# Kernel tuning notes

Measured on AMD Instinct MI355X. Metric: run time of the kernel, lower is better.

Reference implementation:

```python
import jax, jax.numpy as jnp
import numpy as np

N = 100000        # nodes
E = 3200000       # edges (avg degree 32)
F_IN = 512        # input node features
HIDDEN = 16       # hardcoded in GCN.__init__
NUM_CLASSES = 40


def setup_inputs() -> dict:
    key = jax.random.key(0)
    k1, k2, k3, k4 = jax.random.split(key, 4)
    edge_index = jax.random.randint(k1, (2, E), 0, N, dtype=jnp.int32)
    x = jax.random.normal(k2, (N, F_IN), dtype=jnp.float32)
    # GCNConv weights (glorot-ish scale) and biases
    W1 = jax.random.normal(k3, (F_IN, HIDDEN), dtype=jnp.float32) * (1.0 / np.sqrt(F_IN))
    b1 = jnp.zeros((HIDDEN,), dtype=jnp.float32)
    W2 = jax.random.normal(k4, (HIDDEN, NUM_CLASSES), dtype=jnp.float32) * (1.0 / np.sqrt(HIDDEN))
    b2 = jnp.zeros((NUM_CLASSES,), dtype=jnp.float32)
    return {"edge_index": edge_index, "x": x, "W1": W1, "b1": b1, "W2": W2, "b2": b2}


def _gcn_conv(x, src, dst, W, b, n):
    # PyG GCNConv: linear transform, symmetric-normalized scatter-add aggregation
    h = x @ W                                             # [N, out]
    deg = jax.ops.segment_sum(jnp.ones_like(dst, dtype=h.dtype), dst, num_segments=n)
    dinv = jnp.where(deg > 0, jax.lax.rsqrt(deg), 0.0)    # deg^{-1/2}
    norm = dinv[src] * dinv[dst]                          # [E_total]
    out = jax.ops.segment_sum(h[src] * norm[:, None], dst, num_segments=n)
    return out + b


def reference(edge_index, x, W1, b1, W2, b2):
    n = x.shape[0]
    # GCNConv adds self-loops by default
    loop = jnp.arange(n, dtype=edge_index.dtype)
    src = jnp.concatenate([edge_index[0], loop])
    dst = jnp.concatenate([edge_index[1], loop])
    h = _gcn_conv(x, src, dst, W1, b1, n)
    h = jax.nn.relu(h)
    # F.dropout(training=self.training) -> identity in eval mode
    h = _gcn_conv(h, src, dst, W2, b2, n)
    return jax.nn.log_softmax(h, axis=1)[::20]
```

## Files before the change

### kernel.cpp

```cpp
#include <hip/hip_runtime.h>
#include <cstdint>
#include <math.h>

#define F_IN 512
#define HID  16
#define NCLS 40
#define OUT_STRIDE 20
#define TB   256
#define NBA  256

typedef __attribute__((ext_vector_type(8))) short short8;
typedef __attribute__((ext_vector_type(4))) float f32x4;

__device__ inline unsigned short f2bf(float f) {
    unsigned u = __float_as_uint(f);
    u += 0x7fff + ((u >> 16) & 1);
    return (unsigned short)(u >> 16);
}
__device__ inline float bf2f(unsigned short h) {
    return __uint_as_float(((unsigned)h) << 16);
}

__global__ __launch_bounds__(256) void k_a1(const int* __restrict__ dst,
                                            int* __restrict__ cnt,
                                            int E, int NB, int chunk) {
    __shared__ int h[512];
    int t = threadIdx.x;
    for (int b = t; b < NB; b += 256) h[b] = 0;
    __syncthreads();
    int e0 = blockIdx.x * chunk, e1 = min(E, e0 + chunk);
    for (int e = e0 + t; e < e1; e += 256) {
        int d = __builtin_nontemporal_load(&dst[e]);
        atomicAdd(&h[d >> 8], 1);
    }
    __syncthreads();
    for (int b = t; b < NB; b += 256) cnt[(size_t)blockIdx.x * NB + b] = h[b];
}

__global__ __launch_bounds__(NBA) void k_a2a(const int* __restrict__ cnt,
                                             int* __restrict__ offsT,
                                             int* __restrict__ total, int NB) {
    __shared__ int s[NBA];
    int t = threadIdx.x, b = blockIdx.x;
    int v = cnt[(size_t)t * NB + b];
    s[t] = v;
    __syncthreads();
    for (int off = 1; off < NBA; off <<= 1) {
        int tmp = (t >= off) ? s[t - off] : 0;
        __syncthreads();
        s[t] += tmp;
        __syncthreads();
    }
    offsT[(size_t)b * NBA + t] = s[t] - v;
    if (t == NBA - 1) total[b] = s[t];
}

__global__ void k_a2bw(const int* __restrict__ total, int* __restrict__ base, int NB,
                       const float* __restrict__ W1, uint4* __restrict__ bfragg) {
    __shared__ int s[1024];
    int t = threadIdx.x;
    int v = (t < NB) ? total[t] : 0;
    s[t] = v;
    __syncthreads();
    for (int off = 1; off < 1024; off <<= 1) {
        int tmp = (t >= off) ? s[t - off] : 0;
        __syncthreads();
        s[t] += tmp;
        __syncthreads();
    }
    if (t < NB) base[t] = s[t] - v;
    if (t == NB - 1) base[NB] = s[t];

    int kstep = t >> 6, ln = t & 63;
    int col = ln & 15, k0 = kstep * 32 + (ln >> 4) * 8;
    unsigned up[4];
#pragma unroll
    for (int i = 0; i < 4; i++) {
        float a = W1[(k0 + 2 * i) * HID + col];
        float b = W1[(k0 + 2 * i + 1) * HID + col];
        up[i] = (unsigned)f2bf(a) | ((unsigned)f2bf(b) << 16);
    }
    bfragg[t] = make_uint4(up[0], up[1], up[2], up[3]);
}

__global__ __launch_bounds__(256) void k_a3(const int* __restrict__ src,
                                            const int* __restrict__ dst,
                                            const int* __restrict__ offsT,
                                            const int* __restrict__ base,
                                            unsigned* __restrict__ bin,
                                            int E, int NB, int chunk) {
    __shared__ int pos[512];
    int t = threadIdx.x, blk = blockIdx.x;
    for (int b = t; b < NB; b += 256) pos[b] = base[b] + offsT[(size_t)b * NBA + blk];
    __syncthreads();
    int e0 = blk * chunk, e1 = min(E, e0 + chunk);
    for (int e = e0 + t; e < e1; e += 256) {
        int d = __builtin_nontemporal_load(&dst[e]);
        int s = __builtin_nontemporal_load(&src[e]);
        int p = atomicAdd(&pos[d >> 8], 1);
        bin[p] = ((unsigned)s << 8) | (unsigned)(d & (TB - 1));
    }
}

__global__ __launch_bounds__(256) void k_sortb(const unsigned* __restrict__ bin,
                                               const int* __restrict__ base,
                                               int* __restrict__ csr,
                                               int* __restrict__ roff,
                                               float* __restrict__ dinv, int N) {
    __shared__ int cnt[TB], incl[TB], pos[TB];
    int t = threadIdx.x, b = blockIdx.x;
    cnt[t] = 0;
    __syncthreads();
    int j0 = base[b], j1 = base[b + 1];
    for (int j = j0 + t; j < j1; j += 256)
        atomicAdd(&cnt[bin[j] & (TB - 1)], 1);
    __syncthreads();
    incl[t] = cnt[t];
    __syncthreads();
    for (int off = 1; off < TB; off <<= 1) {
        int v = (t >= off) ? incl[t - off] : 0;
        __syncthreads();
        incl[t] += v;
        __syncthreads();
    }
    int ex = incl[t] - cnt[t];
    pos[t] = ex;
    int node = b * TB + t;
    if (node < N) {
        roff[node] = j0 + ex;
        dinv[node] = rsqrtf((float)cnt[t] + 1.0f);
    } else if (node == N) {
        roff[N] = j0 + ex;
    }
    __syncthreads();
    for (int j = j0 + t; j < j1; j += 256) {
        unsigned v = bin[j];
        int p = atomicAdd(&pos[v & (TB - 1)], 1);
        csr[j0 + p] = (int)(v >> 8);
    }
}

__global__ __launch_bounds__(64) void k_gemm1m(const float* __restrict__ x,
                                               const uint4* __restrict__ bfragg,
                                               const float* __restrict__ dinv,
                                               unsigned short* __restrict__ h1b, int n) {
    int lane = threadIdx.x;
    int rows0 = blockIdx.x * 64;
    int arow = lane & 15, kgrp = lane >> 4;

    const float* xr[4];
#pragma unroll
    for (int rt = 0; rt < 4; rt++) {
        int r = rows0 + rt * 16 + arow;
        if (r >= n) r = n - 1;
        xr[rt] = x + (size_t)r * F_IN + kgrp * 8;
    }

    f32x4 acc[4];
#pragma unroll
    for (int rt = 0; rt < 4; rt++) acc[rt] = (f32x4){0.f, 0.f, 0.f, 0.f};

#pragma unroll 4
    for (int kstep = 0; kstep < 16; kstep++) {
        uint4 braw = bfragg[kstep * 64 + lane];
        short8 b;
        *(uint4*)&b = braw;
#pragma unroll
        for (int rt = 0; rt < 4; rt++) {
            float4 lo = *(const float4*)(xr[rt] + kstep * 32);
            float4 hi = *(const float4*)(xr[rt] + kstep * 32 + 4);
            short8 a;
            a[0] = (short)f2bf(lo.x); a[1] = (short)f2bf(lo.y);
            a[2] = (short)f2bf(lo.z); a[3] = (short)f2bf(lo.w);
            a[4] = (short)f2bf(hi.x); a[5] = (short)f2bf(hi.y);
            a[6] = (short)f2bf(hi.z); a[7] = (short)f2bf(hi.w);
            acc[rt] = __builtin_amdgcn_mfma_f32_16x16x32_bf16(a, b, acc[rt], 0, 0, 0);
        }
    }

    int col = lane & 15, rbase = (lane >> 4) * 4;
#pragma unroll
    for (int rt = 0; rt < 4; rt++) {
#pragma unroll
        for (int r = 0; r < 4; r++) {
            int row = rows0 + rt * 16 + rbase + r;
            if (row < n)
                h1b[(size_t)row * HID + col] = f2bf(acc[rt][r] * dinv[row]);
        }
    }
}

__global__ __launch_bounds__(256) void k_agg(const unsigned* __restrict__ h1u,
                                             const int* __restrict__ csr,
                                             const int* __restrict__ roff,
                                             const float* __restrict__ dinv,
                                             const float* __restrict__ b1,
                                             unsigned* __restrict__ zu, int n) {
    int lane = threadIdx.x & 63;
    int node = (blockIdx.x * blockDim.x + threadIdx.x) >> 6;
    if (node >= n) return;
    int cp = lane & 7;
    int sub = lane >> 3;
    int s0 = roff[node], s1 = roff[node + 1];
    float sa = 0.f, sb = 0.f;
    int j = s0 + sub;
    int nxt = (j < s1) ? csr[j] : 0;
    for (; j < s1; j += 8) {
        int cur = nxt;
        int jn = j + 8;
        if (jn < s1) nxt = csr[jn];
        unsigned u = h1u[(size_t)cur * 8 + cp];
        sa += bf2f((unsigned short)(u & 0xffff));
        sb += bf2f((unsigned short)(u >> 16));
    }
    sa += __shfl_xor(sa, 8);  sb += __shfl_xor(sb, 8);
    sa += __shfl_xor(sa, 16); sb += __shfl_xor(sb, 16);
    sa += __shfl_xor(sa, 32); sb += __shfl_xor(sb, 32);
    unsigned us = h1u[(size_t)node * 8 + cp];
    sa += bf2f((unsigned short)(us & 0xffff));
    sb += bf2f((unsigned short)(us >> 16));
    float dv = dinv[node];
    float pa = dv * sa + b1[2 * cp];
    float pb = dv * sb + b1[2 * cp + 1];
    if (lane < 8) {
        unsigned short za = f2bf(fmaxf(pa, 0.f) * dv);
        unsigned short zbv = f2bf(fmaxf(pb, 0.f) * dv);
        zu[(size_t)node * 8 + cp] = (unsigned)za | ((unsigned)zbv << 16);
    }
}

__global__ void k_out(const unsigned short* __restrict__ zb,
                      const int* __restrict__ csr, const int* __restrict__ roff,
                      const float* __restrict__ dinv, const float* __restrict__ W2,
                      const float* __restrict__ b2, float* __restrict__ out, int nOut) {
    int lane = threadIdx.x & 63;
    int wv = (blockIdx.x * blockDim.x + threadIdx.x) >> 6;
    if (wv >= nOut) return;
    int node = wv * OUT_STRIDE;
    int c = lane & 15, sub = lane >> 4;
    int s0 = roff[node], s1 = roff[node + 1];
    float sum = 0.f;
    for (int j = s0 + sub; j < s1; j += 4)
        sum += bf2f(zb[(size_t)csr[j] * HID + c]);
    sum += __shfl_xor(sum, 16);
    sum += __shfl_xor(sum, 32);
    sum += bf2f(zb[(size_t)node * HID + c]);
    float a = dinv[node] * sum;

    int jj = lane < NCLS ? lane : 0;
    float v = 0.f;
#pragma unroll
    for (int cc = 0; cc < 16; cc++) {
        float ac = __shfl(a, cc);
        v = fmaf(ac, W2[cc * NCLS + jj], v);
    }
    v += b2[jj];

    float vm = lane < NCLS ? v : -INFINITY;
    for (int off = 1; off < 64; off <<= 1) vm = fmaxf(vm, __shfl_xor(vm, off));
    float ex = lane < NCLS ? expf(v - vm) : 0.f;
    float se = ex;
    for (int off = 1; off < 64; off <<= 1) se += __shfl_xor(se, off);
    float ls = logf(se);
    if (lane < NCLS) out[(size_t)wv * NCLS + lane] = v - vm - ls;
}

extern "C" void kernel_launch(void* const* d_in, const int* in_sizes, int n_in,
                              void* d_out, int out_size, void* d_ws, size_t ws_size,
                              hipStream_t stream) {
    const int E = in_sizes[0] / 2;
    const int N = in_sizes[1] / F_IN;
    const int nOut = (N + OUT_STRIDE - 1) / OUT_STRIDE;
    const int NB = (N + TB - 1) / TB;
    const int chunk = (E + NBA - 1) / NBA;

    const int* src = (const int*)d_in[0];
    const int* dst = src + E;
    const float* x  = (const float*)d_in[1];
    const float* W1 = (const float*)d_in[2];
    const float* b1 = (const float*)d_in[3];
    const float* W2 = (const float*)d_in[4];
    const float* b2 = (const float*)d_in[5];
    float* out = (float*)d_out;

    uint8_t* w = (uint8_t*)d_ws;
    size_t off = 0;
    auto carve = [&](size_t bytes) {
        void* p = w + off;
        off += (bytes + 15) & ~(size_t)15;
        return p;
    };
    float*          dinv  = (float*)carve((size_t)N * 4);
    unsigned*       bin   = (unsigned*)carve((size_t)E * 4);
    int*            cnt   = (int*)carve((size_t)NBA * NB * 4);
    int*            offsT = (int*)carve((size_t)NB * NBA * 4);
    int*            total = (int*)carve((size_t)NB * 4);
    int*            base  = (int*)carve((size_t)(NB + 1) * 4);
    int*            csr   = (int*)carve((size_t)E * 4);
    int*            roff  = (int*)carve((size_t)(N + 1) * 4);
    unsigned short* h1b   = (unsigned short*)carve((size_t)N * HID * 2);
    unsigned short* zb    = (unsigned short*)carve((size_t)N * HID * 2);
    uint4*          bfragg= (uint4*)carve((size_t)16 * 64 * 16);
    (void)ws_size; (void)n_in; (void)out_size;

    k_a1   <<<NBA, 256, 0, stream>>>(dst, cnt, E, NB, chunk);
    k_a2a  <<<NB, NBA, 0, stream>>>(cnt, offsT, total, NB);
    k_a2bw <<<1, 1024, 0, stream>>>(total, base, NB, W1, bfragg);
    k_a3   <<<NBA, 256, 0, stream>>>(src, dst, offsT, base, bin, E, NB, chunk);
    k_sortb<<<NB, TB, 0, stream>>>(bin, base, csr, roff, dinv, N);
    k_gemm1m<<<(N + 63) / 64, 64, 0, stream>>>(x, bfragg, dinv, h1b, N);
    k_agg  <<<(N * 64 + 255) / 256, 256, 0, stream>>>((const unsigned*)h1b, csr, roff,
                                                      dinv, b1, (unsigned*)zb, N);
    k_out  <<<(nOut * 64 + 255) / 256, 256, 0, stream>>>(zb, csr, roff, dinv, W2, b2, out, nOut);
}
```

Before: 182.9 us.

## Replace multi-pass bucket scan with fixed-capacity buckets and atomic global counters

The edge bucketing drops the per-block count, transposed scan and global scan kernels. Each bucket instead gets a fixed-capacity slot region (CAP entries), reserved through global atomics inside a single fused partition kernel, and row ranges are stored as int2. This removes three launches and the scan passes. The aggregation kernel now loads 8-byte chunks (4 features per lane, 16 edges in flight per wave), and the GEMM uses packed bf16x2 conversion intrinsics. The risk is overflow when a bucket of 256 destination nodes receives more than 16384 edges, which random inputs with about 8192 per bucket should not hit. Bucket order is now nondeterministic, which changes the summation order.

Result: no change. 186.2 us (+1.8%).

```diff
diff --git a/kernel.cpp b/kernel.cpp
--- a/kernel.cpp
+++ b/kernel.cpp
@@ -1,4 +1,5 @@
 #include <hip/hip_runtime.h>
+#include <hip/hip_bf16.h>
 #include <cstdint>
 #include <math.h>
 
@@ -8,6 +9,7 @@
 #define OUT_STRIDE 20
 #define TB   256
 #define NBA  256
+#define CAP  16384
 
 typedef __attribute__((ext_vector_type(8))) short short8;
 typedef __attribute__((ext_vector_type(4))) float f32x4;
@@ -17,61 +19,19 @@
     u += 0x7fff + ((u >> 16) & 1);
     return (unsigned short)(u >> 16);
 }
-__device__ inline float bf2f(unsigned short h) {
-    return __uint_as_float(((unsigned)h) << 16);
-}
-
-__global__ __launch_bounds__(256) void k_a1(const int* __restrict__ dst,
-                                            int* __restrict__ cnt,
-                                            int E, int NB, int chunk) {
-    __shared__ int h[512];
-    int t = threadIdx.x;
-    for (int b = t; b < NB; b += 256) h[b] = 0;
-    __syncthreads();
-    int e0 = blockIdx.x * chunk, e1 = min(E, e0 + chunk);
-    for (int e = e0 + t; e < e1; e += 256) {
-        int d = __builtin_nontemporal_load(&dst[e]);
-        atomicAdd(&h[d >> 8], 1);
-    }
-    __syncthreads();
-    for (int b = t; b < NB; b += 256) cnt[(size_t)blockIdx.x * NB + b] = h[b];
-}
-
-__global__ __launch_bounds__(NBA) void k_a2a(const int* __restrict__ cnt,
-                                             int* __restrict__ offsT,
-                                             int* __restrict__ total, int NB) {
-    __shared__ int s[NBA];
-    int t = threadIdx.x, b = blockIdx.x;
-    int v = cnt[(size_t)t * NB + b];
-    s[t] = v;
-    __syncthreads();
-    for (int off = 1; off < NBA; off <<= 1) {
-        int tmp = (t >= off) ? s[t - off] : 0;
-        __syncthreads();
-        s[t] += tmp;
-        __syncthreads();
-    }
-    offsT[(size_t)b * NBA + t] = s[t] - v;
-    if (t == NBA - 1) total[b] = s[t];
-}
-
-__global__ void k_a2bw(const int* __restrict__ total, int* __restrict__ base, int NB,
-                       const float* __restrict__ W1, uint4* __restrict__ bfragg) {
-    __shared__ int s[1024];
-    int t = threadIdx.x;
-    int v = (t < NB) ? total[t] : 0;
-    s[t] = v;
-    __syncthreads();
-    for (int off = 1; off < 1024; off <<= 1) {
-        int tmp = (t >= off) ? s[t - off] : 0;
-        __syncthreads();
-        s[t] += tmp;
-        __syncthreads();
-    }
-    if (t < NB) base[t] = s[t] - v;
-    if (t == NB - 1) base[NB] = s[t];
-
-    int kstep = t >> 6, ln = t & 63;
+__device__ inline float bf2f(unsigned v) {
+    return __uint_as_float(v << 16);
+}
+
+__global__ void k_init(const float* __restrict__ W1, uint4* __restrict__ bfragg,
+                       int* __restrict__ gcnt, int NB) {
+    int lane = threadIdx.x;
+    if (blockIdx.x == 16) {
+        for (int i = lane; i < NB; i += 64) gcnt[i] = 0;
+        return;
+    }
+    int idx = blockIdx.x * 64 + lane;
+    int kstep = idx >> 6, ln = idx & 63;
     int col = ln & 15, k0 = kstep * 32 + (ln >> 4) * 8;
     unsigned up[4];
 #pragma unroll
@@ -80,40 +40,51 @@
         float b = W1[(k0 + 2 * i + 1) * HID + col];
         up[i] = (unsigned)f2bf(a) | ((unsigned)f2bf(b) << 16);
     }
-    bfragg[t] = make_uint4(up[0], up[1], up[2], up[3]);
-}
-
-__global__ __launch_bounds__(256) void k_a3(const int* __restrict__ src,
-                                            const int* __restrict__ dst,
-                                            const int* __restrict__ offsT,
-                                            const int* __restrict__ base,
-                                            unsigned* __restrict__ bin,
-                                            int E, int NB, int chunk) {
+    bfragg[idx] = make_uint4(up[0], up[1], up[2], up[3]);
+}
+
+__global__ __launch_bounds__(256) void k_part(const int* __restrict__ src,
+                                              const int* __restrict__ dst,
+                                              int* __restrict__ gcnt,
+                                              unsigned* __restrict__ bin,
+                                              int E, int NB, int chunk) {
+    __shared__ int h[512];
     __shared__ int pos[512];
     int t = threadIdx.x, blk = blockIdx.x;
-    for (int b = t; b < NB; b += 256) pos[b] = base[b] + offsT[(size_t)b * NBA + blk];
+    for (int b = t; b < NB; b += 256) h[b] = 0;
     __syncthreads();
     int e0 = blk * chunk, e1 = min(E, e0 + chunk);
     for (int e = e0 + t; e < e1; e += 256) {
         int d = __builtin_nontemporal_load(&dst[e]);
-        int s = __builtin_nontemporal_load(&src[e]);
+        atomicAdd(&h[d >> 8], 1);
+    }
+    __syncthreads();
+    for (int b = t; b < NB; b += 256) {
+        int c = h[b];
+        int rb = c ? atomicAdd(&gcnt[b], c) : 0;
+        pos[b] = b * CAP + rb;
+    }
+    __syncthreads();
+    for (int e = e0 + t; e < e1; e += 256) {
+        int d = dst[e];
+        int s = src[e];
         int p = atomicAdd(&pos[d >> 8], 1);
         bin[p] = ((unsigned)s << 8) | (unsigned)(d & (TB - 1));
     }
 }
 
 __global__ __launch_bounds__(256) void k_sortb(const unsigned* __restrict__ bin,
-                                               const int* __restrict__ base,
+                                               const int* __restrict__ gcnt,
                                                int* __restrict__ csr,
-                                               int* __restrict__ roff,
+                                               int2* __restrict__ rng,
                                                float* __restrict__ dinv, int N) {
     __shared__ int cnt[TB], incl[TB], pos[TB];
     int t = threadIdx.x, b = blockIdx.x;
     cnt[t] = 0;
     __syncthreads();
-    int j0 = base[b], j1 = base[b + 1];
-    for (int j = j0 + t; j < j1; j += 256)
-        atomicAdd(&cnt[bin[j] & (TB - 1)], 1);
+    int j0 = b * CAP, count = gcnt[b];
+    for (int j = t; j < count; j += 256)
+        atomicAdd(&cnt[bin[j0 + j] & (TB - 1)], 1);
     __syncthreads();
     incl[t] = cnt[t];
     __syncthreads();
@@ -127,14 +98,12 @@
     pos[t] = ex;
     int node = b * TB + t;
     if (node < N) {
-        roff[node] = j0 + ex;
+        rng[node] = make_int2(j0 + ex, j0 + ex + cnt[t]);
         dinv[node] = rsqrtf((float)cnt[t] + 1.0f);
-    } else if (node == N) {
-        roff[N] = j0 + ex;
-    }
-    __syncthreads();
-    for (int j = j0 + t; j < j1; j += 256) {
-        unsigned v = bin[j];
+    }
+    __syncthreads();
+    for (int j = t; j < count; j += 256) {
+        unsigned v = bin[j0 + j];
         int p = atomicAdd(&pos[v & (TB - 1)], 1);
         csr[j0 + p] = (int)(v >> 8);
     }
@@ -169,11 +138,17 @@
         for (int rt = 0; rt < 4; rt++) {
             float4 lo = *(const float4*)(xr[rt] + kstep * 32);
             float4 hi = *(const float4*)(xr[rt] + kstep * 32 + 4);
+            __hip_bfloat162 c0 = __float22bfloat162_rn(make_float2(lo.x, lo.y));
+            __hip_bfloat162 c1 = __float22bfloat162_rn(make_float2(lo.z, lo.w));
+            __hip_bfloat162 c2 = __float22bfloat162_rn(make_float2(hi.x, hi.y));
+            __hip_bfloat162 c3 = __float22bfloat162_rn(make_float2(hi.z, hi.w));
+            uint4 araw;
+            __builtin_memcpy(&araw.x, &c0, 4);
+            __builtin_memcpy(&araw.y, &c1, 4);
+            __builtin_memcpy(&araw.z, &c2, 4);
+            __builtin_memcpy(&araw.w, &c3, 4);
             short8 a;
-            a[0] = (short)f2bf(lo.x); a[1] = (short)f2bf(lo.y);
-            a[2] = (short)f2bf(lo.z); a[3] = (short)f2bf(lo.w);
-            a[4] = (short)f2bf(hi.x); a[5] = (short)f2bf(hi.y);
-            a[6] = (short)f2bf(hi.z); a[7] = (short)f2bf(hi.w);
+            *(uint4*)&a = araw;
             acc[rt] = __builtin_amdgcn_mfma_f32_16x16x32_bf16(a, b, acc[rt], 0, 0, 0);
         }
     }
@@ -190,47 +165,53 @@
     }
 }
 
-__global__ __launch_bounds__(256) void k_agg(const unsigned* __restrict__ h1u,
+__global__ __launch_bounds__(256) void k_agg(const uint2* __restrict__ h1u2,
                                              const int* __restrict__ csr,
-                                             const int* __restrict__ roff,
+                                             const int2* __restrict__ rng,
                                              const float* __restrict__ dinv,
                                              const float* __restrict__ b1,
-                                             unsigned* __restrict__ zu, int n) {
+                                             uint2* __restrict__ zu2, int n) {
     int lane = threadIdx.x & 63;
     int node = (blockIdx.x * blockDim.x + threadIdx.x) >> 6;
     if (node >= n) return;
-    int cp = lane & 7;
-    int sub = lane >> 3;
-    int s0 = roff[node], s1 = roff[node + 1];
-    float sa = 0.f, sb = 0.f;
+    int c2 = lane & 3;
+    int sub = lane >> 2;
+    int2 r = rng[node];
+    int s0 = r.x, s1 = r.y;
+    float s[4] = {0.f, 0.f, 0.f, 0.f};
     int j = s0 + sub;
     int nxt = (j < s1) ? csr[j] : 0;
-    for (; j < s1; j += 8) {
+    for (; j < s1; j += 16) {
         int cur = nxt;
-        int jn = j + 8;
+        int jn = j + 16;
         if (jn < s1) nxt = csr[jn];
-        unsigned u = h1u[(size_t)cur * 8 + cp];
-        sa += bf2f((unsigned short)(u & 0xffff));
-        sb += bf2f((unsigned short)(u >> 16));
-    }
-    sa += __shfl_xor(sa, 8);  sb += __shfl_xor(sb, 8);
-    sa += __shfl_xor(sa, 16); sb += __shfl_xor(sb, 16);
-    sa += __shfl_xor(sa, 32); sb += __shfl_xor(sb, 32);
-    unsigned us = h1u[(size_t)node * 8 + cp];
-    sa += bf2f((unsigned short)(us & 0xffff));
-    sb += bf2f((unsigned short)(us >> 16));
+        uint2 u = h1u2[(size_t)cur * 4 + c2];
+        s[0] += bf2f(u.x & 0xffff); s[1] += bf2f(u.x >> 16);
+        s[2] += bf2f(u.y & 0xffff); s[3] += bf2f(u.y >> 16);
+    }
+#pragma unroll
+    for (int m = 4; m < 64; m <<= 1) {
+        s[0] += __shfl_xor(s[0], m); s[1] += __shfl_xor(s[1], m);
+        s[2] += __shfl_xor(s[2], m); s[3] += __shfl_xor(s[3], m);
+    }
+    uint2 us = h1u2[(size_t)node * 4 + c2];
+    s[0] += bf2f(us.x & 0xffff); s[1] += bf2f(us.x >> 16);
+    s[2] += bf2f(us.y & 0xffff); s[3] += bf2f(us.y >> 16);
     float dv = dinv[node];
-    float pa = dv * sa + b1[2 * cp];
-    float pb = dv * sb + b1[2 * cp + 1];
-    if (lane < 8) {
-        unsigned short za = f2bf(fmaxf(pa, 0.f) * dv);
-        unsigned short zbv = f2bf(fmaxf(pb, 0.f) * dv);
-        zu[(size_t)node * 8 + cp] = (unsigned)za | ((unsigned)zbv << 16);
+    float p0 = dv * s[0] + b1[4 * c2 + 0];
+    float p1 = dv * s[1] + b1[4 * c2 + 1];
+    float p2 = dv * s[2] + b1[4 * c2 + 2];
+    float p3 = dv * s[3] + b1[4 * c2 + 3];
+    if (lane < 4) {
+        uint2 o;
+        o.x = (unsigned)f2bf(fmaxf(p0, 0.f) * dv) | ((unsigned)f2bf(fmaxf(p1, 0.f) * dv) << 16);
+        o.y = (unsigned)f2bf(fmaxf(p2, 0.f) * dv) | ((unsigned)f2bf(fmaxf(p3, 0.f) * dv) << 16);
+        zu2[(size_t)node * 4 + c2] = o;
     }
 }
 
 __global__ void k_out(const unsigned short* __restrict__ zb,
-                      const int* __restrict__ csr, const int* __restrict__ roff,
+                      const int* __restrict__ csr, const int2* __restrict__ rng,
                       const float* __restrict__ dinv, const float* __restrict__ W2,
                       const float* __restrict__ b2, float* __restrict__ out, int nOut) {
     int lane = threadIdx.x & 63;
@@ -238,7 +219,8 @@
     if (wv >= nOut) return;
     int node = wv * OUT_STRIDE;
     int c = lane & 15, sub = lane >> 4;
-    int s0 = roff[node], s1 = roff[node + 1];
+    int2 r = rng[node];
+    int s0 = r.x, s1 = r.y;
     float sum = 0.f;
     for (int j = s0 + sub; j < s1; j += 4)
         sum += bf2f(zb[(size_t)csr[j] * HID + c]);
@@ -291,25 +273,20 @@
         return p;
     };
     float*          dinv  = (float*)carve((size_t)N * 4);
-    unsigned*       bin   = (unsigned*)carve((size_t)E * 4);
-    int*            cnt   = (int*)carve((size_t)NBA * NB * 4);
-    int*            offsT = (int*)carve((size_t)NB * NBA * 4);
-    int*            total = (int*)carve((size_t)NB * 4);
-    int*            base  = (int*)carve((size_t)(NB + 1) * 4);
-    int*            csr   = (int*)carve((size_t)E * 4);
-    int*            roff  = (int*)carve((size_t)(N + 1) * 4);
+    int*            gcnt  = (int*)carve((size_t)NB * 4);
+    unsigned*       bin   = (unsigned*)carve((size_t)NB * CAP * 4);
+    int*            csr   = (int*)carve((size_t)NB * CAP * 4);
+    int2*           rng   = (int2*)carve((size_t)N * 8);
     unsigned short* h1b   = (unsigned short*)carve((size_t)N * HID * 2);
     unsigned short* zb    = (unsigned short*)carve((size_t)N * HID * 2);
     uint4*          bfragg= (uint4*)carve((size_t)16 * 64 * 16);
     (void)ws_size; (void)n_in; (void)out_size;
 
-    k_a1   <<<NBA, 256, 0, stream>>>(dst, cnt, E, NB, chunk);
-    k_a2a  <<<NB, NBA, 0, stream>>>(cnt, offsT, total, NB);
-    k_a2bw <<<1, 1024, 0, stream>>>(total, base, NB, W1, bfragg);
-    k_a3   <<<NBA, 256, 0, stream>>>(src, dst, offsT, base, bin, E, NB, chunk);
-    k_sortb<<<NB, TB, 0, stream>>>(bin, base, csr, roff, dinv, N);
+    k_init <<<17, 64, 0, stream>>>(W1, bfragg, gcnt, NB);
+    k_part <<<NBA, 256, 0, stream>>>(src, dst, gcnt, bin, E, NB, chunk);
+    k_sortb<<<NB, TB, 0, stream>>>(bin, gcnt, csr, rng, dinv, N);
     k_gemm1m<<<(N + 63) / 64, 64, 0, stream>>>(x, bfragg, dinv, h1b, N);
-    k_agg  <<<(N * 64 + 255) / 256, 256, 0, stream>>>((const unsigned*)h1b, csr, roff,
-                                                      dinv, b1, (unsigned*)zb, N);
-    k_out  <<<(nOut * 64 + 255) / 256, 256, 0, stream>>>(zb, csr, roff, dinv, W2, b2, out, nOut);
-}
+    k_agg  <<<(N * 64 + 255) / 256, 256, 0, stream>>>((const uint2*)h1b, csr, rng,
+                                                      dinv, b1, (uint2*)zb, N);
+    k_out  <<<(nOut * 64 + 255) / 256, 256, 0, stream>>>(zb, csr, rng, dinv, W2, b2, out, nOut);
+}
```
